# Kernel tuning notes

Measured on AMD Instinct MI355X. Metric: run time of the kernel, lower is better.

Reference implementation:

```python
import jax, jax.numpy as jnp
import numpy as np

N, C, H, W = 16, 64, 128, 128
KH, KW = 3, 3
SH, SW = 1, 1


def _window_flat_indices(H, W):
    """Flat input indices of each element of each sliding window.
    Returns int32 array [num_windows, KH*KW]."""
    Ho = (H - KH) // SH + 1
    Wo = (W - KW) // SW + 1
    i = np.arange(Ho) * SH
    j = np.arange(Wo) * SW
    a = np.arange(KH)
    b = np.arange(KW)
    rows = i[:, None, None, None] + a[None, None, :, None]   # [Ho,1,KH,1]
    cols = j[None, :, None, None] + b[None, None, None, :]   # [1,Wo,1,KW]
    flat = (rows * W + cols).reshape(Ho * Wo, KH * KW)       # [Wn, K]
    return jnp.asarray(flat, dtype=jnp.int32)


def setup_inputs() -> dict:
    key = jax.random.key(0)
    x = jax.random.normal(key, (N, C, H, W), dtype=jnp.float32)
    return {"x": x}


def reference(x):
    n, c, h, w = x.shape
    flat = _window_flat_indices(h, w)            # [Wn, K]
    Wn, K = flat.shape
    nc = n * c
    xf = x.reshape(nc, h * w)                    # [NC, HW]
    patches = xf[:, flat]                        # [NC, Wn, K]
    amax = jnp.argmax(patches, axis=-1)          # [NC, Wn] local winner
    amin = jnp.argmin(patches, axis=-1)          # [NC, Wn]
    warp = jnp.arange(Wn)[None, :]
    win_max = flat[warp, amax]                   # [NC, Wn] flat input idx of max winner
    win_min = flat[warp, amin]                   # [NC, Wn]
    idx = jnp.concatenate([win_max, win_min], axis=1)                      # [NC, 2Wn]
    vals = jnp.concatenate([jnp.ones((Wn,), x.dtype), -jnp.ones((Wn,), x.dtype)])
    counts = jnp.zeros((nc, h * w), x.dtype)
    counts = counts.at[jnp.arange(nc)[:, None], idx].add(vals[None, :])
    return counts.reshape(n, c, h, w)
```

## Files before the change

### kernel.cpp

```cpp
#include <hip/hip_runtime.h>


#define HH 128
#define WW 128
#define HO 126
#define WO 126
#define NWIN (HO * WO)
#define PLANE (HH * WW)
#define NPLANES (16 * 64)
#define BLOCK 1024

__global__ __launch_bounds__(BLOCK, 8)
void energy_pool2d_kernel(const float* __restrict__ x, float* __restrict__ out) {
    __shared__ int cnt[PLANE];

    const int tid = threadIdx.x;
    const int plane = blockIdx.x;
    const float* __restrict__ xp = x + (size_t)plane * PLANE;

    int4* c4 = (int4*)cnt;
#pragma unroll
    for (int i = 0; i < PLANE / 4 / BLOCK; ++i) {
        c4[tid + i * BLOCK] = make_int4(0, 0, 0, 0);
    }
    __syncthreads();

    for (int w = tid; w < NWIN; w += BLOCK) {
        const int wi = w / WO;
        const int wj = w - wi * WO;
        const float* __restrict__ p = xp + wi * WW + wj;

        float v0 = p[0],        v1 = p[1],          v2 = p[2];
        float v3 = p[WW],       v4 = p[WW + 1],     v5 = p[WW + 2];
        float v6 = p[2 * WW],   v7 = p[2 * WW + 1], v8 = p[2 * WW + 2];

        float vmax = v0, vmin = v0;
        int omax = 0, omin = 0;
#define STEP(val, off)                                        \
        do {                                                  \
            if ((val) > vmax) { vmax = (val); omax = (off); } \
            if ((val) < vmin) { vmin = (val); omin = (off); } \
        } while (0)
        STEP(v1, 1);
        STEP(v2, 2);
        STEP(v3, WW);
        STEP(v4, WW + 1);
        STEP(v5, WW + 2);
        STEP(v6, 2 * WW);
        STEP(v7, 2 * WW + 1);
        STEP(v8, 2 * WW + 2);
#undef STEP

        const int base = wi * WW + wj;
        atomicAdd(&cnt[base + omax], 1);
        atomicAdd(&cnt[base + omin], -1);
    }
    __syncthreads();

    float4* __restrict__ o4 = (float4*)(out + (size_t)plane * PLANE);
#pragma unroll
    for (int i = 0; i < PLANE / 4 / BLOCK; ++i) {
        const int4 ci = c4[tid + i * BLOCK];
        o4[tid + i * BLOCK] =
            make_float4((float)ci.x, (float)ci.y, (float)ci.z, (float)ci.w);
    }
}

extern "C" void kernel_launch(void* const* d_in, const int* in_sizes, int n_in,
                              void* d_out, int out_size, void* d_ws, size_t ws_size,
                              hipStream_t stream) {
    const float* x = (const float*)d_in[0];
    float* out = (float*)d_out;
    energy_pool2d_kernel<<<NPLANES, BLOCK, 0, stream>>>(x, out);
}
```

Before: 40.00 us.

## Reuse per-row horizontal max/min across vertical window strips

Each thread now owns a column and walks a strip of up to 16 output rows. It computes the row-wise 3-wide max/min once per input row and keeps the last three in a rolling register buffer, so vertically adjacent windows share them. This cuts redundant global loads and comparisons from nine per window to about three, and removes the division and modulo in the indexing. The cost is that 2 of every 128 lanes sit idle, and the last group handles 14 rows while the others handle 16. Ties are still resolved by first occurrence in row-major order, matching the reference argmax/argmin.

```diff
diff --git a/kernel.cpp b/kernel.cpp
--- a/kernel.cpp
+++ b/kernel.cpp
@@ -5,10 +5,45 @@
 #define WW 128
 #define HO 126
 #define WO 126
-#define NWIN (HO * WO)
 #define PLANE (HH * WW)
 #define NPLANES (16 * 64)
 #define BLOCK 1024
+#define GT 128
+#define GROUPS (BLOCK / GT)
+#define ROWS_PER_G 16
+
+__device__ __forceinline__ void hstat(const float* __restrict__ p, int base,
+                                      float& M, int& A, float& m, int& a) {
+    const float v0 = p[0], v1 = p[1], v2 = p[2];
+    M = v0; A = base;
+    if (v1 > M) { M = v1; A = base + 1; }
+    if (v2 > M) { M = v2; A = base + 2; }
+    m = v0; a = base;
+    if (v1 < m) { m = v1; a = base + 1; }
+    if (v2 < m) { m = v2; a = base + 2; }
+}
+
+template <int NWR>
+__device__ __forceinline__ void run_rows(const float* __restrict__ p, int base,
+                                         int* __restrict__ cnt) {
+    float M[3], m[3];
+    int A[3], a[3];
+    hstat(p, base, M[0], A[0], m[0], a[0]); p += WW; base += WW;
+    hstat(p, base, M[1], A[1], m[1], a[1]); p += WW; base += WW;
+#pragma unroll
+    for (int r = 0; r < NWR; ++r) {
+        const int s0 = r % 3, s1 = (r + 1) % 3, s2 = (r + 2) % 3;
+        hstat(p, base, M[s2], A[s2], m[s2], a[s2]); p += WW; base += WW;
+        float WM = M[s0]; int wf = A[s0];
+        if (M[s1] > WM) { WM = M[s1]; wf = A[s1]; }
+        if (M[s2] > WM) { WM = M[s2]; wf = A[s2]; }
+        atomicAdd(&cnt[wf], 1);
+        float Wm = m[s0]; int wg = a[s0];
+        if (m[s1] < Wm) { Wm = m[s1]; wg = a[s1]; }
+        if (m[s2] < Wm) { Wm = m[s2]; wg = a[s2]; }
+        atomicAdd(&cnt[wg], -1);
+    }
+}
 
 __global__ __launch_bounds__(BLOCK, 8)
 void energy_pool2d_kernel(const float* __restrict__ x, float* __restrict__ out) {
@@ -20,40 +55,20 @@
 
     int4* c4 = (int4*)cnt;
 #pragma unroll
-    for (int i = 0; i < PLANE / 4 / BLOCK; ++i) {
+    for (int i = 0; i < PLANE / 4 / BLOCK; ++i)
         c4[tid + i * BLOCK] = make_int4(0, 0, 0, 0);
-    }
     __syncthreads();
 
-    for (int w = tid; w < NWIN; w += BLOCK) {
-        const int wi = w / WO;
-        const int wj = w - wi * WO;
-        const float* __restrict__ p = xp + wi * WW + wj;
-
-        float v0 = p[0],        v1 = p[1],          v2 = p[2];
-        float v3 = p[WW],       v4 = p[WW + 1],     v5 = p[WW + 2];
-        float v6 = p[2 * WW],   v7 = p[2 * WW + 1], v8 = p[2 * WW + 2];
-
-        float vmax = v0, vmin = v0;
-        int omax = 0, omin = 0;
-#define STEP(val, off)                                        \
-        do {                                                  \
-            if ((val) > vmax) { vmax = (val); omax = (off); } \
-            if ((val) < vmin) { vmin = (val); omin = (off); } \
-        } while (0)
-        STEP(v1, 1);
-        STEP(v2, 2);
-        STEP(v3, WW);
-        STEP(v4, WW + 1);
-        STEP(v5, WW + 2);
-        STEP(v6, 2 * WW);
-        STEP(v7, 2 * WW + 1);
-        STEP(v8, 2 * WW + 2);
-#undef STEP
-
-        const int base = wi * WW + wj;
-        atomicAdd(&cnt[base + omax], 1);
-        atomicAdd(&cnt[base + omin], -1);
+    const int g = tid >> 7;
+    const int t = tid & (GT - 1);
+    if (t < WO) {
+        const int wr0 = g * ROWS_PER_G;
+        const int base = wr0 * WW + t;
+        const float* __restrict__ p = xp + base;
+        if (g < GROUPS - 1)
+            run_rows<ROWS_PER_G>(p, base, cnt);
+        else
+            run_rows<HO - (GROUPS - 1) * ROWS_PER_G>(p, base, cnt);
     }
     __syncthreads();
 
```

Measured after the change: 64.80 us. 1.62x slower.

## Process 2x4 window tiles per thread with float4 register reuse

Applied to the files above, without the earlier changes.

Each thread now handles a 2-row by 4-column tile of windows, loading a 4x8 input patch with float4 vector loads and reusing the values across the eight overlapping 3x3 windows. This replaces nine scalar loads per window plus a division per window, aiming to cut global load instructions and index arithmetic. The last column tile processes only two windows and skips the out-of-range loads. The cost is higher register pressure and fewer active threads per block, since there are 2016 tiles for 1024 threads.

```diff
diff --git a/kernel.cpp b/kernel.cpp
--- a/kernel.cpp
+++ b/kernel.cpp
@@ -5,10 +5,36 @@
 #define WW 128
 #define HO 126
 #define WO 126
-#define NWIN (HO * WO)
 #define PLANE (HH * WW)
 #define NPLANES (16 * 64)
 #define BLOCK 1024
+#define CTILES 32
+#define RTILES 63
+#define NTILES (CTILES * RTILES)
+
+__device__ __forceinline__ void scan9(float w0, float w1, float w2,
+                                      float w3, float w4, float w5,
+                                      float w6, float w7, float w8,
+                                      int base, int* __restrict__ cnt) {
+    float vmax = w0, vmin = w0;
+    int omax = 0, omin = 0;
+#define STEP(v, off)                                      \
+    do {                                                  \
+        if ((v) > vmax) { vmax = (v); omax = (off); }     \
+        if ((v) < vmin) { vmin = (v); omin = (off); }     \
+    } while (0)
+    STEP(w1, 1);
+    STEP(w2, 2);
+    STEP(w3, WW);
+    STEP(w4, WW + 1);
+    STEP(w5, WW + 2);
+    STEP(w6, 2 * WW);
+    STEP(w7, 2 * WW + 1);
+    STEP(w8, 2 * WW + 2);
+#undef STEP
+    atomicAdd(&cnt[base + omax], 1);
+    atomicAdd(&cnt[base + omin], -1);
+}
 
 __global__ __launch_bounds__(BLOCK, 8)
 void energy_pool2d_kernel(const float* __restrict__ x, float* __restrict__ out) {
@@ -20,40 +46,48 @@
 
     int4* c4 = (int4*)cnt;
 #pragma unroll
-    for (int i = 0; i < PLANE / 4 / BLOCK; ++i) {
+    for (int i = 0; i < PLANE / 4 / BLOCK; ++i)
         c4[tid + i * BLOCK] = make_int4(0, 0, 0, 0);
-    }
     __syncthreads();
 
-    for (int w = tid; w < NWIN; w += BLOCK) {
-        const int wi = w / WO;
-        const int wj = w - wi * WO;
-        const float* __restrict__ p = xp + wi * WW + wj;
+    for (int t = tid; t < NTILES; t += BLOCK) {
+        const int rt = t >> 5;
+        const int ct = t & 31;
+        const int wr0 = rt * 2;
+        const int j0 = ct * 4;
+        const float* __restrict__ p = xp + wr0 * WW + j0;
 
-        float v0 = p[0],        v1 = p[1],          v2 = p[2];
-        float v3 = p[WW],       v4 = p[WW + 1],     v5 = p[WW + 2];
-        float v6 = p[2 * WW],   v7 = p[2 * WW + 1], v8 = p[2 * WW + 2];
+        const float4 a0 = *(const float4*)(p);
+        const float4 a1 = *(const float4*)(p + WW);
+        const float4 a2 = *(const float4*)(p + 2 * WW);
+        const float4 a3 = *(const float4*)(p + 3 * WW);
+        float4 b0, b1, b2, b3;
+        if (ct < CTILES - 1) {
+            b0 = *(const float4*)(p + 4);
+            b1 = *(const float4*)(p + WW + 4);
+            b2 = *(const float4*)(p + 2 * WW + 4);
+            b3 = *(const float4*)(p + 3 * WW + 4);
+        } else {
+            b0 = b1 = b2 = b3 = make_float4(0.f, 0.f, 0.f, 0.f);
+        }
+        const float r0[8] = {a0.x, a0.y, a0.z, a0.w, b0.x, b0.y, b0.z, b0.w};
+        const float r1[8] = {a1.x, a1.y, a1.z, a1.w, b1.x, b1.y, b1.z, b1.w};
+        const float r2[8] = {a2.x, a2.y, a2.z, a2.w, b2.x, b2.y, b2.z, b2.w};
+        const float r3[8] = {a3.x, a3.y, a3.z, a3.w, b3.x, b3.y, b3.z, b3.w};
 
-        float vmax = v0, vmin = v0;
-        int omax = 0, omin = 0;
-#define STEP(val, off)                                        \
-        do {                                                  \
-            if ((val) > vmax) { vmax = (val); omax = (off); } \
-            if ((val) < vmin) { vmin = (val); omin = (off); } \
-        } while (0)
-        STEP(v1, 1);
-        STEP(v2, 2);
-        STEP(v3, WW);
-        STEP(v4, WW + 1);
-        STEP(v5, WW + 2);
-        STEP(v6, 2 * WW);
-        STEP(v7, 2 * WW + 1);
-        STEP(v8, 2 * WW + 2);
-#undef STEP
-
-        const int base = wi * WW + wj;
-        atomicAdd(&cnt[base + omax], 1);
-        atomicAdd(&cnt[base + omin], -1);
+        const int nw = (ct < CTILES - 1) ? 4 : 2;
+        const int base0 = wr0 * WW + j0;
+#pragma unroll
+        for (int c = 0; c < 4; ++c) {
+            if (c < nw) {
+                scan9(r0[c], r0[c + 1], r0[c + 2],
+                      r1[c], r1[c + 1], r1[c + 2],
+                      r2[c], r2[c + 1], r2[c + 2], base0 + c, cnt);
+                scan9(r1[c], r1[c + 1], r1[c + 2],
+                      r2[c], r2[c + 1], r2[c + 2],
+                      r3[c], r3[c + 1], r3[c + 2], base0 + WW + c, cnt);
+            }
+        }
     }
     __syncthreads();
 
```

Measured after the change: 32.22 us. 19.5% less time.

## Compute 4x4 window tiles per thread with separable row-then-column argmax

Applied to the files above, without the earlier changes.

Each thread now owns a 4x4 tile of output windows and loads a 6x8 register patch with float4 loads, where before it loaded 9 scalars for every window in a strided loop. Max and min winners are found separably: horizontal 3-wide reductions per row, then vertical 3-wide reductions over the row results. This shares loads and comparisons across neighbouring windows and removes the per-window division. Tie-breaking relies on first-index-of-equal ordering, and edge tiles clamp their loads and mask invalid windows. NaN inputs may behave differently because fmaxf is used instead of strict comparisons.

```diff
diff --git a/kernel.cpp b/kernel.cpp
--- a/kernel.cpp
+++ b/kernel.cpp
@@ -5,7 +5,6 @@
 #define WW 128
 #define HO 126
 #define WO 126
-#define NWIN (HO * WO)
 #define PLANE (HH * WW)
 #define NPLANES (16 * 64)
 #define BLOCK 1024
@@ -20,40 +19,65 @@
 
     int4* c4 = (int4*)cnt;
 #pragma unroll
-    for (int i = 0; i < PLANE / 4 / BLOCK; ++i) {
+    for (int i = 0; i < PLANE / 4 / BLOCK; ++i)
         c4[tid + i * BLOCK] = make_int4(0, 0, 0, 0);
-    }
     __syncthreads();
 
-    for (int w = tid; w < NWIN; w += BLOCK) {
-        const int wi = w / WO;
-        const int wj = w - wi * WO;
-        const float* __restrict__ p = xp + wi * WW + wj;
+    const int rt = tid >> 5;
+    const int ct = tid & 31;
+    const int wr0 = rt * 4;
+    const int j0 = ct * 4;
+    const bool cfull = (ct < 31);
+    const bool rfull = (rt < 31);
+    const int base = wr0 * WW + j0;
+    const float* __restrict__ p = xp + base;
 
-        float v0 = p[0],        v1 = p[1],          v2 = p[2];
-        float v3 = p[WW],       v4 = p[WW + 1],     v5 = p[WW + 2];
-        float v6 = p[2 * WW],   v7 = p[2 * WW + 1], v8 = p[2 * WW + 2];
+    float r[6][8];
+#pragma unroll
+    for (int q = 0; q < 6; ++q) {
+        const int qs = (q >= 4 && !rfull) ? 3 : q;
+        const float* rowp = p + qs * WW;
+        const float4 a = *(const float4*)(rowp);
+        const float4 b = *(const float4*)(rowp + (cfull ? 4 : 0));
+        r[q][0] = a.x; r[q][1] = a.y; r[q][2] = a.z; r[q][3] = a.w;
+        r[q][4] = b.x; r[q][5] = b.y; r[q][6] = b.z; r[q][7] = b.w;
+    }
 
-        float vmax = v0, vmin = v0;
-        int omax = 0, omin = 0;
-#define STEP(val, off)                                        \
-        do {                                                  \
-            if ((val) > vmax) { vmax = (val); omax = (off); } \
-            if ((val) < vmin) { vmin = (val); omin = (off); } \
-        } while (0)
-        STEP(v1, 1);
-        STEP(v2, 2);
-        STEP(v3, WW);
-        STEP(v4, WW + 1);
-        STEP(v5, WW + 2);
-        STEP(v6, 2 * WW);
-        STEP(v7, 2 * WW + 1);
-        STEP(v8, 2 * WW + 2);
-#undef STEP
-
-        const int base = wi * WW + wj;
-        atomicAdd(&cnt[base + omax], 1);
-        atomicAdd(&cnt[base + omin], -1);
+#pragma unroll
+    for (int o = 0; o < 4; ++o) {
+        float hM[6], hm[6];
+        int hA[6], ha[6];
+#pragma unroll
+        for (int q = 0; q < 6; ++q) {
+            const float v0 = r[q][o], v1 = r[q][o + 1], v2 = r[q][o + 2];
+            const int f0 = q * WW + o;
+            float M = fmaxf(fmaxf(v0, v1), v2);
+            int A = f0 + 2;
+            if (v1 == M) A = f0 + 1;
+            if (v0 == M) A = f0;
+            float m = fminf(fminf(v0, v1), v2);
+            int a = f0 + 2;
+            if (v1 == m) a = f0 + 1;
+            if (v0 == m) a = f0;
+            hM[q] = M; hA[q] = A; hm[q] = m; ha[q] = a;
+        }
+        const bool oval = (o < 2) || cfull;
+#pragma unroll
+        for (int q = 0; q < 4; ++q) {
+            const bool qval = (q < 2) || rfull;
+            if (oval && qval) {
+                const float WM = fmaxf(fmaxf(hM[q], hM[q + 1]), hM[q + 2]);
+                int wA = hA[q + 2];
+                if (hM[q + 1] == WM) wA = hA[q + 1];
+                if (hM[q] == WM) wA = hA[q];
+                const float Wm = fminf(fminf(hm[q], hm[q + 1]), hm[q + 2]);
+                int wa = ha[q + 2];
+                if (hm[q + 1] == Wm) wa = ha[q + 1];
+                if (hm[q] == Wm) wa = ha[q];
+                atomicAdd(&cnt[base + wA], 1);
+                atomicAdd(&cnt[base + wa], -1);
+            }
+        }
     }
     __syncthreads();
 
```

Result: faster. 38.33 us (-4.2%).
